# Performance work log

Hardware: AMD Instinct MI355X
Metric: run time of the kernel (lower is better)

The kernel has to match this reference:

```python
import jax, jax.numpy as jnp
import numpy as np

NUM_GROUPS = 16
EPS = 1e-6


def setup_inputs() -> dict:
    key = jax.random.key(0)
    k1, k2, k3, k4 = jax.random.split(key, 4)
    B, N = 16, 131072
    pred = jax.random.normal(k1, (B, N, 3), dtype=jnp.float32)
    target = jax.random.normal(k2, (B, N, 3), dtype=jnp.float32)
    mask = jax.random.randint(k3, (B, N), 0, 2, dtype=jnp.int32)
    groups = jax.random.randint(k4, (B, N), 0, NUM_GROUPS, dtype=jnp.int32)
    return {"pred": pred, "target": target, "mask": mask, "groups": groups}


def _group_median_normalizer(z, valid, groups):
    """Per-point depth normalizer: lower-median of |z| within each (batch, group)
    over valid points, clamped to EPS; groups with no valid points get 1.0.
    z, valid, groups: (B, N). Returns (B, N)."""
    gids = jnp.arange(NUM_GROUPS, dtype=groups.dtype)
    in_g = (groups[:, None, :] == gids[None, :, None]) & valid[:, None, :]  # (B,G,N)
    inf = jnp.asarray(jnp.inf, z.dtype)
    z_g = jnp.where(in_g, z[:, None, :], inf)        # (B,G,N), invalid -> +inf
    z_sorted = jnp.sort(z_g, axis=-1)                # valid values occupy first cnt slots
    cnt = jnp.sum(in_g, axis=-1)                     # (B,G)
    idx = jnp.maximum(cnt - 1, 0) // 2               # torch lower median index
    med = jnp.take_along_axis(z_sorted, idx[..., None], axis=-1)[..., 0]  # (B,G)
    # empty groups give +inf -> nan_to_num -> 1.0, matching torch's untouched default
    med = jnp.nan_to_num(med, nan=1.0, posinf=1.0, neginf=1.0)
    med_safe = jnp.maximum(jnp.abs(med), EPS)        # clamp(|median|, min=eps)
    return jnp.take_along_axis(med_safe, groups, axis=-1)  # gather per point (B,N)


def _log_transform(x):
    return jnp.sign(x) * jnp.log1p(jnp.abs(x))


def reference(pred, target, mask, groups):
    valid = mask.astype(bool)                        # (B,N)
    # shared depth normalization: denominator from TARGET, used for both
    norm = _group_median_normalizer(target[..., 2], valid, groups)  # (B,N)
    vm = valid[..., None]                            # (B,N,1)
    inv = 1.0 / norm[..., None]
    p = jnp.nan_to_num(jnp.where(vm, pred, 0.0) * inv, nan=0.0, posinf=0.0, neginf=0.0)
    t = jnp.nan_to_num(jnp.where(vm, target, 0.0) * inv, nan=0.0, posinf=0.0, neginf=0.0)
    loss = jnp.abs(_log_transform(p) - _log_transform(t))  # (B,N,3)
    loss = jnp.where(vm, loss, 0.0)
    denom = 3.0 * jnp.sum(valid).astype(jnp.float32) + 1e-6  # expanded mask count
    return jnp.sum(loss) / denom
```

## Files before the change

### kernel.cpp

```cpp
#include <hip/hip_runtime.h>
#include <math.h>

#define NPTS_N 131072
#define NGROUP 16
#define NBG 256
#define CBLK 512
#define BPB 32
#define SEGCAP 256
#define NSEL 6144
#define EPSF 1e-6f

__device__ __forceinline__ unsigned f2key(float f) {
    unsigned u = __float_as_uint(f);
    return (u & 0x80000000u) ? ~u : (u | 0x80000000u);
}
__device__ __forceinline__ float key2f(unsigned k) {
    unsigned u = (k & 0x80000000u) ? (k ^ 0x80000000u) : ~k;
    return __uint_as_float(u);
}
__device__ __forceinline__ float flog1p(float a) {
    return __log2f(1.0f + a) * 0.69314718056f;
}

__global__ __launch_bounds__(256) void compact_kernel(
        const float* __restrict__ target,
        const int* __restrict__ mask,
        const int* __restrict__ groups,
        unsigned* __restrict__ bucket,
        unsigned* __restrict__ blockCnt) {
    __shared__ unsigned scnt[NGROUP];
    int tid = threadIdx.x;
    int blk = blockIdx.x;
    int base = blk * 4096;
    if (tid < NGROUP) scnt[tid] = 0;
    __syncthreads();
    unsigned keys[16]; unsigned meta[16]; unsigned vbits = 0;
    #pragma unroll
    for (int k = 0; k < 4; ++k) {
        int i = base + k * 1024 + tid * 4;
        int4 m4 = *(const int4*)(mask + i);
        int4 g4 = *(const int4*)(groups + i);
        int mm[4] = {m4.x, m4.y, m4.z, m4.w};
        int gg[4] = {g4.x, g4.y, g4.z, g4.w};
        #pragma unroll
        for (int j = 0; j < 4; ++j) {
            int idx = k * 4 + j;
            if (mm[j]) {
                keys[idx] = f2key(target[(size_t)(i + j) * 3 + 2]);
                unsigned pos = atomicAdd(&scnt[gg[j]], 1u);
                meta[idx] = ((unsigned)gg[j] << 16) | pos;
                vbits |= 1u << idx;
            }
        }
    }
    __syncthreads();
    if (tid < NGROUP) blockCnt[blk * NGROUP + tid] = scnt[tid];
    #pragma unroll
    for (int idx = 0; idx < 16; ++idx) {
        if (vbits & (1u << idx)) {
            unsigned g = meta[idx] >> 16, pos = meta[idx] & 0xFFFFu;
            if (pos < SEGCAP)
                bucket[((size_t)(blk * NGROUP + g)) * SEGCAP + pos] = keys[idx];
        }
    }
}

__global__ __launch_bounds__(256) void select_kernel(
        const unsigned* __restrict__ bucket,
        const unsigned* __restrict__ blockCnt,
        float* __restrict__ norm,
        unsigned* __restrict__ cnt) {
    __shared__ unsigned skey[NSEL];
    __shared__ unsigned hist[2048];
    __shared__ unsigned sc[BPB];
    __shared__ unsigned segoff[BPB + 1];
    __shared__ unsigned wsum[4];
    __shared__ unsigned sres[2];
    int bg = blockIdx.x, tid = threadIdx.x;
    int b = bg >> 4, g = bg & 15;
    if (tid < BPB) sc[tid] = blockCnt[(b * BPB + tid) * NGROUP + g];
    __syncthreads();
    if (tid == 0) {
        unsigned o = 0;
        for (int c = 0; c < BPB; ++c) { segoff[c] = o; o += sc[c]; }
        segoff[BPB] = o;
    }
    __syncthreads();
    unsigned ntrue = segoff[BPB];
    unsigned n = ntrue > NSEL ? NSEL : ntrue;
    if (tid == 0) cnt[bg] = ntrue;
    if (n == 0) { if (tid == 0) norm[bg] = 1.0f; return; }
    for (int c = 0; c < BPB; ++c) {
        unsigned count = sc[c], o = segoff[c];
        const unsigned* src = bucket + ((size_t)((b * BPB + c) * NGROUP + g)) * SEGCAP;
        for (unsigned j = tid; j < count; j += 256)
            if (o + j < NSEL) skey[o + j] = src[j];
    }
    __syncthreads();

    unsigned rank = (n - 1) >> 1;
    unsigned selkey = 0;
    const int shifts[3] = {21, 10, 0};
    const int widths[3] = {11, 11, 10};
    for (int p = 0; p < 3; ++p) {
        int sh = shifts[p], w = widths[p];
        unsigned nb = 1u << w, bmask = nb - 1;
        for (unsigned j = tid; j < nb; j += 256) hist[j] = 0;
        __syncthreads();
        for (unsigned j = tid; j < n; j += 256) {
            unsigned key = skey[j];
            bool in = (p == 0) || ((key >> (sh + w)) == selkey);
            if (in) atomicAdd(&hist[(key >> sh) & bmask], 1u);
        }
        __syncthreads();
        unsigned cpl = nb >> 8;
        unsigned basebin = tid * cpl;
        unsigned s = 0;
        for (unsigned j = 0; j < cpl; ++j) s += hist[basebin + j];
        unsigned inc = s;
        #pragma unroll
        for (int o = 1; o < 64; o <<= 1) {
            unsigned v = __shfl_up(inc, o, 64);
            if ((tid & 63) >= o) inc += v;
        }
        if ((tid & 63) == 63) wsum[tid >> 6] = inc;
        __syncthreads();
        unsigned woff = 0;
        for (int w2 = 0; w2 < (tid >> 6); ++w2) woff += wsum[w2];
        unsigned excl = woff + inc - s;
        if (rank >= excl && rank < excl + s) {
            unsigned run = excl, binSel = basebin;
            for (unsigned j = 0; j < cpl; ++j) {
                unsigned h = hist[basebin + j];
                if (run + h > rank) { binSel = basebin + j; break; }
                run += h;
            }
            sres[0] = binSel; sres[1] = rank - run;
        }
        __syncthreads();
        selkey = (selkey << w) | sres[0];
        rank = sres[1];
    }
    if (tid == 0) norm[bg] = fmaxf(fabsf(key2f(selkey)), EPSF);
}

__global__ __launch_bounds__(256) void loss_kernel(
        const float* __restrict__ pred,
        const float* __restrict__ target,
        const int* __restrict__ mask,
        const int* __restrict__ groups,
        const float* __restrict__ norm,
        float* __restrict__ partials) {
    __shared__ float sinv[NGROUP];
    __shared__ float swsum[4];
    int tid = threadIdx.x;
    int b = blockIdx.x >> 7;
    if (tid < NGROUP) sinv[tid] = 1.0f / norm[(b << 4) + tid];
    __syncthreads();
    int p0 = b * NPTS_N + (blockIdx.x & 127) * 1024 + tid * 4;
    const float4* pr4 = (const float4*)(pred + (size_t)p0 * 3);
    const float4* tg4 = (const float4*)(target + (size_t)p0 * 3);
    int4 m4 = *(const int4*)(mask + p0);
    int4 g4 = *(const int4*)(groups + p0);
    float pv[12], tv[12];
    *(float4*)(pv + 0) = pr4[0]; *(float4*)(pv + 4) = pr4[1]; *(float4*)(pv + 8) = pr4[2];
    *(float4*)(tv + 0) = tg4[0]; *(float4*)(tv + 4) = tg4[1]; *(float4*)(tv + 8) = tg4[2];
    int mm[4] = {m4.x, m4.y, m4.z, m4.w};
    int gg[4] = {g4.x, g4.y, g4.z, g4.w};
    float acc = 0.f;
    #pragma unroll
    for (int k = 0; k < 4; ++k) {
        if (mm[k]) {
            float inv = sinv[gg[k] & 15];
            #pragma unroll
            for (int c = 0; c < 3; ++c) {
                float pp = pv[k * 3 + c] * inv;
                float tt = tv[k * 3 + c] * inv;
                float lp = copysignf(flog1p(fabsf(pp)), pp);
                float lt = copysignf(flog1p(fabsf(tt)), tt);
                acc += fabsf(lp - lt);
            }
        }
    }
    #pragma unroll
    for (int off = 32; off; off >>= 1) acc += __shfl_down(acc, off, 64);
    if ((tid & 63) == 0) swsum[tid >> 6] = acc;
    __syncthreads();
    if (tid == 0) partials[blockIdx.x] = swsum[0] + swsum[1] + swsum[2] + swsum[3];
}

__global__ __launch_bounds__(256) void finalize_kernel(
        const float* __restrict__ partials,
        const unsigned* __restrict__ cnt,
        float* __restrict__ out) {
    __shared__ float sred[256];
    int tid = threadIdx.x;
    float s = 0.f;
    for (int j = tid; j < 2048; j += 256) s += partials[j];
    sred[tid] = s; __syncthreads();
    for (int st = 128; st; st >>= 1) { if (tid < st) sred[tid] += sred[tid + st]; __syncthreads(); }
    float total = sred[0];
    __syncthreads();
    sred[tid] = (float)cnt[tid]; __syncthreads();
    for (int st = 128; st; st >>= 1) { if (tid < st) sred[tid] += sred[tid + st]; __syncthreads(); }
    if (tid == 0) out[0] = total / (3.0f * sred[0] + 1e-6f);
}

extern "C" void kernel_launch(void* const* d_in, const int* in_sizes, int n_in,
                              void* d_out, int out_size, void* d_ws, size_t ws_size,
                              hipStream_t stream) {
    const float* pred   = (const float*)d_in[0];
    const float* target = (const float*)d_in[1];
    const int*   mask   = (const int*)d_in[2];
    const int*   groups = (const int*)d_in[3];
    float* out = (float*)d_out;

    char* ws = (char*)d_ws;
    const size_t BUCKET_BYTES = (size_t)CBLK * NGROUP * SEGCAP * sizeof(unsigned);
    unsigned* bucket   = (unsigned*)ws;
    unsigned* blockCnt = (unsigned*)(ws + BUCKET_BYTES);
    unsigned* cnt      = (unsigned*)(ws + BUCKET_BYTES + 32768);
    float*    norm     = (float*)(ws + BUCKET_BYTES + 32768 + 1024);
    float*    partials = (float*)(ws + BUCKET_BYTES + 32768 + 2048);

    compact_kernel<<<dim3(CBLK), dim3(256), 0, stream>>>(target, mask, groups, bucket, blockCnt);
    select_kernel<<<dim3(NBG), dim3(256), 0, stream>>>(bucket, blockCnt, norm, cnt);
    loss_kernel<<<dim3(2048), dim3(256), 0, stream>>>(pred, target, mask, groups, norm, partials);
    finalize_kernel<<<dim3(1), dim3(256), 0, stream>>>(partials, cnt, out);
}
```

Baseline: 138.5 us.

## Fuse compact, select, loss and finalize into one cooperative grid-synced kernel

The four separate kernel launches become a single cooperative kernel of 1024 blocks. The phases are separated by grid.sync(), and each block handles 2048 points. Bucketing now uses 64 blocks per batch with a segment capacity of 192, and shared memory is reused through a union across phases. This removes launch gaps and inter-kernel drain, at the cost of three grid-wide barriers and a select phase where only 256 of the 1024 blocks do any work.

```diff
diff --git a/kernel.cpp b/kernel.cpp
--- a/kernel.cpp
+++ b/kernel.cpp
@@ -1,12 +1,16 @@
 #include <hip/hip_runtime.h>
+#include <hip/hip_cooperative_groups.h>
 #include <math.h>
+
+namespace cg = cooperative_groups;
 
 #define NPTS_N 131072
 #define NGROUP 16
 #define NBG 256
-#define CBLK 512
-#define BPB 32
-#define SEGCAP 256
+#define GRID_B 1024
+#define PPB 2048
+#define BPB 64
+#define SEGCAP 192
 #define NSEL 6144
 #define EPSF 1e-6f
 
@@ -22,188 +26,203 @@
     return __log2f(1.0f + a) * 0.69314718056f;
 }
 
-__global__ __launch_bounds__(256) void compact_kernel(
+struct SelSh {
+    unsigned skey[NSEL];
+    unsigned hist[2048];
+    unsigned sc[BPB];
+    unsigned segoff[BPB + 1];
+    unsigned wsum[4];
+    unsigned sres[2];
+};
+struct MiscSh {
+    unsigned scnt[NGROUP];
+    float    sinv[NGROUP];
+    float    swsum[4];
+    float    red[256];
+};
+
+__global__ __launch_bounds__(256, 4) void fused_kernel(
+        const float* __restrict__ pred,
         const float* __restrict__ target,
         const int* __restrict__ mask,
         const int* __restrict__ groups,
         unsigned* __restrict__ bucket,
-        unsigned* __restrict__ blockCnt) {
-    __shared__ unsigned scnt[NGROUP];
+        unsigned* __restrict__ blockCnt,
+        unsigned* __restrict__ cnt,
+        float* __restrict__ norm,
+        float* __restrict__ partials,
+        float* __restrict__ out) {
+    __shared__ union { SelSh sel; MiscSh misc; } sh;
+    cg::grid_group grid = cg::this_grid();
     int tid = threadIdx.x;
     int blk = blockIdx.x;
-    int base = blk * 4096;
-    if (tid < NGROUP) scnt[tid] = 0;
-    __syncthreads();
-    unsigned keys[16]; unsigned meta[16]; unsigned vbits = 0;
-    #pragma unroll
-    for (int k = 0; k < 4; ++k) {
-        int i = base + k * 1024 + tid * 4;
-        int4 m4 = *(const int4*)(mask + i);
-        int4 g4 = *(const int4*)(groups + i);
-        int mm[4] = {m4.x, m4.y, m4.z, m4.w};
-        int gg[4] = {g4.x, g4.y, g4.z, g4.w};
-        #pragma unroll
-        for (int j = 0; j < 4; ++j) {
-            int idx = k * 4 + j;
-            if (mm[j]) {
-                keys[idx] = f2key(target[(size_t)(i + j) * 3 + 2]);
-                unsigned pos = atomicAdd(&scnt[gg[j]], 1u);
-                meta[idx] = ((unsigned)gg[j] << 16) | pos;
-                vbits |= 1u << idx;
-            }
-        }
-    }
-    __syncthreads();
-    if (tid < NGROUP) blockCnt[blk * NGROUP + tid] = scnt[tid];
-    #pragma unroll
-    for (int idx = 0; idx < 16; ++idx) {
-        if (vbits & (1u << idx)) {
-            unsigned g = meta[idx] >> 16, pos = meta[idx] & 0xFFFFu;
-            if (pos < SEGCAP)
-                bucket[((size_t)(blk * NGROUP + g)) * SEGCAP + pos] = keys[idx];
-        }
-    }
-}
-
-__global__ __launch_bounds__(256) void select_kernel(
-        const unsigned* __restrict__ bucket,
-        const unsigned* __restrict__ blockCnt,
-        float* __restrict__ norm,
-        unsigned* __restrict__ cnt) {
-    __shared__ unsigned skey[NSEL];
-    __shared__ unsigned hist[2048];
-    __shared__ unsigned sc[BPB];
-    __shared__ unsigned segoff[BPB + 1];
-    __shared__ unsigned wsum[4];
-    __shared__ unsigned sres[2];
-    int bg = blockIdx.x, tid = threadIdx.x;
-    int b = bg >> 4, g = bg & 15;
-    if (tid < BPB) sc[tid] = blockCnt[(b * BPB + tid) * NGROUP + g];
-    __syncthreads();
-    if (tid == 0) {
-        unsigned o = 0;
-        for (int c = 0; c < BPB; ++c) { segoff[c] = o; o += sc[c]; }
-        segoff[BPB] = o;
-    }
-    __syncthreads();
-    unsigned ntrue = segoff[BPB];
-    unsigned n = ntrue > NSEL ? NSEL : ntrue;
-    if (tid == 0) cnt[bg] = ntrue;
-    if (n == 0) { if (tid == 0) norm[bg] = 1.0f; return; }
-    for (int c = 0; c < BPB; ++c) {
-        unsigned count = sc[c], o = segoff[c];
-        const unsigned* src = bucket + ((size_t)((b * BPB + c) * NGROUP + g)) * SEGCAP;
-        for (unsigned j = tid; j < count; j += 256)
-            if (o + j < NSEL) skey[o + j] = src[j];
-    }
-    __syncthreads();
-
-    unsigned rank = (n - 1) >> 1;
-    unsigned selkey = 0;
-    const int shifts[3] = {21, 10, 0};
-    const int widths[3] = {11, 11, 10};
-    for (int p = 0; p < 3; ++p) {
-        int sh = shifts[p], w = widths[p];
-        unsigned nb = 1u << w, bmask = nb - 1;
-        for (unsigned j = tid; j < nb; j += 256) hist[j] = 0;
-        __syncthreads();
-        for (unsigned j = tid; j < n; j += 256) {
-            unsigned key = skey[j];
-            bool in = (p == 0) || ((key >> (sh + w)) == selkey);
-            if (in) atomicAdd(&hist[(key >> sh) & bmask], 1u);
-        }
-        __syncthreads();
-        unsigned cpl = nb >> 8;
-        unsigned basebin = tid * cpl;
-        unsigned s = 0;
-        for (unsigned j = 0; j < cpl; ++j) s += hist[basebin + j];
-        unsigned inc = s;
-        #pragma unroll
-        for (int o = 1; o < 64; o <<= 1) {
-            unsigned v = __shfl_up(inc, o, 64);
-            if ((tid & 63) >= o) inc += v;
-        }
-        if ((tid & 63) == 63) wsum[tid >> 6] = inc;
-        __syncthreads();
-        unsigned woff = 0;
-        for (int w2 = 0; w2 < (tid >> 6); ++w2) woff += wsum[w2];
-        unsigned excl = woff + inc - s;
-        if (rank >= excl && rank < excl + s) {
-            unsigned run = excl, binSel = basebin;
-            for (unsigned j = 0; j < cpl; ++j) {
-                unsigned h = hist[basebin + j];
-                if (run + h > rank) { binSel = basebin + j; break; }
-                run += h;
-            }
-            sres[0] = binSel; sres[1] = rank - run;
-        }
-        __syncthreads();
-        selkey = (selkey << w) | sres[0];
-        rank = sres[1];
-    }
-    if (tid == 0) norm[bg] = fmaxf(fabsf(key2f(selkey)), EPSF);
-}
-
-__global__ __launch_bounds__(256) void loss_kernel(
-        const float* __restrict__ pred,
-        const float* __restrict__ target,
-        const int* __restrict__ mask,
-        const int* __restrict__ groups,
-        const float* __restrict__ norm,
-        float* __restrict__ partials) {
-    __shared__ float sinv[NGROUP];
-    __shared__ float swsum[4];
-    int tid = threadIdx.x;
-    int b = blockIdx.x >> 7;
-    if (tid < NGROUP) sinv[tid] = 1.0f / norm[(b << 4) + tid];
-    __syncthreads();
-    int p0 = b * NPTS_N + (blockIdx.x & 127) * 1024 + tid * 4;
-    const float4* pr4 = (const float4*)(pred + (size_t)p0 * 3);
-    const float4* tg4 = (const float4*)(target + (size_t)p0 * 3);
-    int4 m4 = *(const int4*)(mask + p0);
-    int4 g4 = *(const int4*)(groups + p0);
-    float pv[12], tv[12];
-    *(float4*)(pv + 0) = pr4[0]; *(float4*)(pv + 4) = pr4[1]; *(float4*)(pv + 8) = pr4[2];
-    *(float4*)(tv + 0) = tg4[0]; *(float4*)(tv + 4) = tg4[1]; *(float4*)(tv + 8) = tg4[2];
-    int mm[4] = {m4.x, m4.y, m4.z, m4.w};
-    int gg[4] = {g4.x, g4.y, g4.z, g4.w};
-    float acc = 0.f;
-    #pragma unroll
-    for (int k = 0; k < 4; ++k) {
-        if (mm[k]) {
-            float inv = sinv[gg[k] & 15];
+
+    {
+        if (tid < NGROUP) sh.misc.scnt[tid] = 0;
+        __syncthreads();
+        int base = blk * PPB;
+        unsigned segbase = (unsigned)blk * NGROUP;
+        #pragma unroll
+        for (int k = 0; k < 2; ++k) {
+            int i = base + k * 1024 + tid * 4;
+            int4 m4 = *(const int4*)(mask + i);
+            int4 g4 = *(const int4*)(groups + i);
+            int mm[4] = {m4.x, m4.y, m4.z, m4.w};
+            int gg[4] = {g4.x, g4.y, g4.z, g4.w};
             #pragma unroll
-            for (int c = 0; c < 3; ++c) {
-                float pp = pv[k * 3 + c] * inv;
-                float tt = tv[k * 3 + c] * inv;
-                float lp = copysignf(flog1p(fabsf(pp)), pp);
-                float lt = copysignf(flog1p(fabsf(tt)), tt);
-                acc += fabsf(lp - lt);
-            }
-        }
-    }
-    #pragma unroll
-    for (int off = 32; off; off >>= 1) acc += __shfl_down(acc, off, 64);
-    if ((tid & 63) == 0) swsum[tid >> 6] = acc;
-    __syncthreads();
-    if (tid == 0) partials[blockIdx.x] = swsum[0] + swsum[1] + swsum[2] + swsum[3];
-}
-
-__global__ __launch_bounds__(256) void finalize_kernel(
-        const float* __restrict__ partials,
-        const unsigned* __restrict__ cnt,
-        float* __restrict__ out) {
-    __shared__ float sred[256];
-    int tid = threadIdx.x;
-    float s = 0.f;
-    for (int j = tid; j < 2048; j += 256) s += partials[j];
-    sred[tid] = s; __syncthreads();
-    for (int st = 128; st; st >>= 1) { if (tid < st) sred[tid] += sred[tid + st]; __syncthreads(); }
-    float total = sred[0];
-    __syncthreads();
-    sred[tid] = (float)cnt[tid]; __syncthreads();
-    for (int st = 128; st; st >>= 1) { if (tid < st) sred[tid] += sred[tid + st]; __syncthreads(); }
-    if (tid == 0) out[0] = total / (3.0f * sred[0] + 1e-6f);
+            for (int j = 0; j < 4; ++j) {
+                if (mm[j]) {
+                    unsigned key = f2key(target[(size_t)(i + j) * 3 + 2]);
+                    unsigned pos = atomicAdd(&sh.misc.scnt[gg[j]], 1u);
+                    if (pos < SEGCAP)
+                        bucket[(size_t)(segbase + gg[j]) * SEGCAP + pos] = key;
+                }
+            }
+        }
+        __syncthreads();
+        if (tid < NGROUP) blockCnt[blk * NGROUP + tid] = sh.misc.scnt[tid];
+    }
+    grid.sync();
+
+    if (blk < NBG) {
+        int b = blk >> 4, g = blk & 15;
+        if (tid < BPB) {
+            unsigned s = blockCnt[(b * BPB + tid) * NGROUP + g];
+            sh.sel.sc[tid] = s;
+            unsigned inc = s;
+            #pragma unroll
+            for (int o = 1; o < 64; o <<= 1) {
+                unsigned v = __shfl_up(inc, o, 64);
+                if (tid >= o) inc += v;
+            }
+            sh.sel.segoff[tid + 1] = inc;
+            if (tid == 0) sh.sel.segoff[0] = 0;
+        }
+        __syncthreads();
+        unsigned ntrue = sh.sel.segoff[BPB];
+        unsigned n = ntrue > NSEL ? NSEL : ntrue;
+        if (tid == 0) cnt[blk] = ntrue;
+        if (n == 0) {
+            if (tid == 0) norm[blk] = 1.0f;
+        } else {
+            int wv = tid >> 6, ln = tid & 63;
+            for (int c = wv; c < BPB; c += 4) {
+                unsigned count = sh.sel.sc[c], o = sh.sel.segoff[c];
+                if (count > SEGCAP) count = SEGCAP;
+                const unsigned* src = bucket + (size_t)((b * BPB + c) * NGROUP + g) * SEGCAP;
+                for (unsigned j = ln; j < count; j += 64)
+                    if (o + j < NSEL) sh.sel.skey[o + j] = src[j];
+            }
+            __syncthreads();
+
+            unsigned rank = (n - 1) >> 1;
+            unsigned selkey = 0;
+            const int shifts[3] = {21, 10, 0};
+            const int widths[3] = {11, 11, 10};
+            for (int p = 0; p < 3; ++p) {
+                int sft = shifts[p], w = widths[p];
+                unsigned nb = 1u << w, bmask = nb - 1;
+                for (unsigned j = tid; j < nb; j += 256) sh.sel.hist[j] = 0;
+                __syncthreads();
+                for (unsigned j = tid; j < n; j += 256) {
+                    unsigned key = sh.sel.skey[j];
+                    bool in = (p == 0) || ((key >> (sft + w)) == selkey);
+                    if (in) atomicAdd(&sh.sel.hist[(key >> sft) & bmask], 1u);
+                }
+                __syncthreads();
+                unsigned cpl = nb >> 8;
+                unsigned basebin = tid * cpl;
+                unsigned s = 0;
+                for (unsigned j = 0; j < cpl; ++j) s += sh.sel.hist[basebin + j];
+                unsigned inc = s;
+                #pragma unroll
+                for (int o = 1; o < 64; o <<= 1) {
+                    unsigned v = __shfl_up(inc, o, 64);
+                    if ((tid & 63) >= o) inc += v;
+                }
+                if ((tid & 63) == 63) sh.sel.wsum[tid >> 6] = inc;
+                __syncthreads();
+                unsigned woff = 0;
+                for (int w2 = 0; w2 < (tid >> 6); ++w2) woff += sh.sel.wsum[w2];
+                unsigned excl = woff + inc - s;
+                if (rank >= excl && rank < excl + s) {
+                    unsigned run = excl, binSel = basebin;
+                    for (unsigned j = 0; j < cpl; ++j) {
+                        unsigned h = sh.sel.hist[basebin + j];
+                        if (run + h > rank) { binSel = basebin + j; break; }
+                        run += h;
+                    }
+                    sh.sel.sres[0] = binSel; sh.sel.sres[1] = rank - run;
+                }
+                __syncthreads();
+                selkey = (selkey << w) | sh.sel.sres[0];
+                rank = sh.sel.sres[1];
+                __syncthreads();
+            }
+            if (tid == 0) norm[blk] = fmaxf(fabsf(key2f(selkey)), EPSF);
+        }
+    }
+    grid.sync();
+
+    {
+        int b = blk >> 6;
+        if (tid < NGROUP) sh.misc.sinv[tid] = 1.0f / norm[(b << 4) + tid];
+        __syncthreads();
+        int base = blk * PPB;
+        float acc = 0.f;
+        #pragma unroll
+        for (int k = 0; k < 2; ++k) {
+            int p0 = base + k * 1024 + tid * 4;
+            const float4* pr4 = (const float4*)(pred + (size_t)p0 * 3);
+            const float4* tg4 = (const float4*)(target + (size_t)p0 * 3);
+            int4 m4 = *(const int4*)(mask + p0);
+            int4 g4 = *(const int4*)(groups + p0);
+            float pv[12], tv[12];
+            *(float4*)(pv + 0) = pr4[0]; *(float4*)(pv + 4) = pr4[1]; *(float4*)(pv + 8) = pr4[2];
+            *(float4*)(tv + 0) = tg4[0]; *(float4*)(tv + 4) = tg4[1]; *(float4*)(tv + 8) = tg4[2];
+            int mm[4] = {m4.x, m4.y, m4.z, m4.w};
+            int gg[4] = {g4.x, g4.y, g4.z, g4.w};
+            #pragma unroll
+            for (int q = 0; q < 4; ++q) {
+                if (mm[q]) {
+                    float inv = sh.misc.sinv[gg[q] & 15];
+                    #pragma unroll
+                    for (int c = 0; c < 3; ++c) {
+                        float pp = pv[q * 3 + c] * inv;
+                        float tt = tv[q * 3 + c] * inv;
+                        float lp = copysignf(flog1p(fabsf(pp)), pp);
+                        float lt = copysignf(flog1p(fabsf(tt)), tt);
+                        acc += fabsf(lp - lt);
+                    }
+                }
+            }
+        }
+        #pragma unroll
+        for (int off = 32; off; off >>= 1) acc += __shfl_down(acc, off, 64);
+        if ((tid & 63) == 0) sh.misc.swsum[tid >> 6] = acc;
+        __syncthreads();
+        if (tid == 0)
+            partials[blk] = sh.misc.swsum[0] + sh.misc.swsum[1] + sh.misc.swsum[2] + sh.misc.swsum[3];
+    }
+    grid.sync();
+
+    if (blk == 0) {
+        float s = 0.f;
+        #pragma unroll
+        for (int j = 0; j < 4; ++j) s += partials[tid + j * 256];
+        sh.misc.red[tid] = s; __syncthreads();
+        for (int st = 128; st; st >>= 1) {
+            if (tid < st) sh.misc.red[tid] += sh.misc.red[tid + st];
+            __syncthreads();
+        }
+        float total = sh.misc.red[0]; __syncthreads();
+        sh.misc.red[tid] = (float)cnt[tid]; __syncthreads();
+        for (int st = 128; st; st >>= 1) {
+            if (tid < st) sh.misc.red[tid] += sh.misc.red[tid + st];
+            __syncthreads();
+        }
+        if (tid == 0) out[0] = total / (3.0f * sh.misc.red[0] + 1e-6f);
+    }
 }
 
 extern "C" void kernel_launch(void* const* d_in, const int* in_sizes, int n_in,
@@ -216,15 +235,16 @@
     float* out = (float*)d_out;
 
     char* ws = (char*)d_ws;
-    const size_t BUCKET_BYTES = (size_t)CBLK * NGROUP * SEGCAP * sizeof(unsigned);
+    const size_t BUCKET_BYTES = (size_t)GRID_B * NGROUP * SEGCAP * sizeof(unsigned);
     unsigned* bucket   = (unsigned*)ws;
     unsigned* blockCnt = (unsigned*)(ws + BUCKET_BYTES);
-    unsigned* cnt      = (unsigned*)(ws + BUCKET_BYTES + 32768);
-    float*    norm     = (float*)(ws + BUCKET_BYTES + 32768 + 1024);
-    float*    partials = (float*)(ws + BUCKET_BYTES + 32768 + 2048);
-
-    compact_kernel<<<dim3(CBLK), dim3(256), 0, stream>>>(target, mask, groups, bucket, blockCnt);
-    select_kernel<<<dim3(NBG), dim3(256), 0, stream>>>(bucket, blockCnt, norm, cnt);
-    loss_kernel<<<dim3(2048), dim3(256), 0, stream>>>(pred, target, mask, groups, norm, partials);
-    finalize_kernel<<<dim3(1), dim3(256), 0, stream>>>(partials, cnt, out);
-}
+    unsigned* cnt      = (unsigned*)(ws + BUCKET_BYTES + 65536);
+    float*    normv    = (float*)(ws + BUCKET_BYTES + 65536 + 1024);
+    float*    partials = (float*)(ws + BUCKET_BYTES + 65536 + 2048);
+
+    void* args[] = {(void*)&pred, (void*)&target, (void*)&mask, (void*)&groups,
+                    (void*)&bucket, (void*)&blockCnt, (void*)&cnt, (void*)&normv,
+                    (void*)&partials, (void*)&out};
+    hipLaunchCooperativeKernel((void*)fused_kernel, dim3(GRID_B), dim3(256),
+                               args, 0, stream);
+}
```

After: 439.0 us. 217% more time.
